# Optimization experiments

Hardware: AMD Instinct MI355X
Metric: run time of the kernel (lower is better)

## Reference

```python
import jax, jax.numpy as jnp
import numpy as np


def setup_inputs() -> dict:
    key = jax.random.key(0)
    k1, k2 = jax.random.split(key)
    B, N, P = 8, 16384, 2048
    xyz = jax.random.uniform(k1, (B, N, 3), dtype=jnp.float32)
    center_xyz = jax.random.uniform(k2, (B, P, 3), dtype=jnp.float32)
    return {
        "xyz": xyz,
        "center_xyz": center_xyz,
        "max_radius": jnp.float32(0.2),
        "sample_num": 32,
    }


def reference(xyz, center_xyz, max_radius, sample_num):
    # xyz: [B, N, 3], center_xyz: [B, P, 3] -> idx: [B, P, sample_num] int32
    B, P, _ = center_xyz.shape
    N = xyz.shape[1]
    S = int(sample_num)

    # squared distances via ||c||^2 + ||x||^2 - 2 c.x (avoids [B,P,N,3] temp)
    xn = jnp.sum(xyz * xyz, axis=-1)                      # [B, N]
    cn = jnp.sum(center_xyz * center_xyz, axis=-1)        # [B, P]
    dot = jnp.einsum("bpd,bnd->bpn", center_xyz, xyz)     # [B, P, N]
    d2 = cn[:, :, None] + xn[:, None, :] - 2.0 * dot       # [B, P, N]

    mask = d2 < (max_radius * max_radius)                  # dist < r  <=>  dist^2 < r^2
    # rank of each point among the valid ones (in index order), as in torch.where order
    rank = jnp.cumsum(mask.astype(jnp.int32), axis=-1) - 1 # [B, P, N]
    take = mask & (rank < S)
    # valid points write into slot=rank; everything else into dump slot S (discarded)
    slot = jnp.where(take, rank, S)                        # [B, P, N]

    buf = jnp.zeros((B, P, S + 1), dtype=jnp.int32)        # zeros match torch init fill
    bi = jnp.arange(B)[:, None, None]
    pi = jnp.arange(P)[None, :, None]
    src = jnp.broadcast_to(jnp.arange(N, dtype=jnp.int32), (B, P, N))
    buf = buf.at[bi, pi, slot].set(src)
    return buf[:, :, :S]
```

## Files before the change

kernel.cpp:

```cpp
#include <hip/hip_runtime.h>
#include <hip/hip_bf16.h>


typedef float f32x4 __attribute__((ext_vector_type(4)));

__global__ __launch_bounds__(256) void pack_points(
    const float* __restrict__ xyz,
    f32x4* __restrict__ q,
    int total)
{
    const int n = blockIdx.x * blockDim.x + threadIdx.x;
    if (n >= total) return;
    const float x = xyz[(size_t)n * 3 + 0];
    const float y = xyz[(size_t)n * 3 + 1];
    const float z = xyz[(size_t)n * 3 + 2];
    const float xn = __builtin_fmaf(z, z,
                      __builtin_fmaf(y, y, __fmul_rn(x, x)));
    f32x4 v;
    v[0] = x; v[1] = y; v[2] = z; v[3] = xn;
    q[n] = v;
}

__global__ __launch_bounds__(256) void ball_query_block(
    const f32x4* __restrict__ q,
    const float* __restrict__ center,
    const float* __restrict__ p_radius,
    const int*   __restrict__ p_sample,
    int* __restrict__ out,
    int B, int N, int P)
{
    const int S = p_sample[0];
    const float r = p_radius[0];
    const float r2 = __fmul_rn(r, r);

    const int c = blockIdx.x;
    const int lane = threadIdx.x & 63;
    const int wv = threadIdx.x >> 6;

    const int b = c / P;

    const float cx = center[(size_t)c * 3 + 0];
    const float cy = center[(size_t)c * 3 + 1];
    const float cz = center[(size_t)c * 3 + 2];
    const float cn = __builtin_fmaf(cz, cz,
                      __builtin_fmaf(cy, cy, __fmul_rn(cx, cx)));

    const f32x4* qb = q + (size_t)b * N;
    int* ob = out + (size_t)c * S;

    __shared__ int counts[2][4];

    int cnt = 0;
    int buf = 0;
    for (int n0 = 0; n0 < N; n0 += 1024) {
        const int base = n0 + wv * 256 + lane;

        f32x4 v[4];
#pragma unroll
        for (int j = 0; j < 4; ++j) {
            v[j] = qb[base + j * 64];
        }

        unsigned long long mm[4];
        int pc[4];
        int wtotal = 0;
#pragma unroll
        for (int j = 0; j < 4; ++j) {
            const float x = v[j][0], y = v[j][1], z = v[j][2];
            const float xn = v[j][3];
            const float dot = __builtin_fmaf(cz, z,
                               __builtin_fmaf(cy, y, __fmul_rn(cx, x)));
            const float d2 = __fsub_rn(__fadd_rn(cn, xn), __fmul_rn(2.0f, dot));
            mm[j] = __ballot(d2 < r2);
            pc[j] = __popcll(mm[j]);
            wtotal += pc[j];
        }

        if (lane == 0) counts[buf][wv] = wtotal;
        __syncthreads();

        const int c0 = counts[buf][0];
        const int c1 = counts[buf][1];
        const int c2 = counts[buf][2];
        const int c3 = counts[buf][3];
        int prefix = 0;
        if (wv > 0) prefix += c0;
        if (wv > 1) prefix += c1;
        if (wv > 2) prefix += c2;
        const int total = (c0 + c1) + (c2 + c3);

        if (wtotal != 0) {
            int off = cnt + prefix;
#pragma unroll
            for (int j = 0; j < 4; ++j) {
                const unsigned long long m = mm[j];
                const bool valid = (m >> lane) & 1ull;
                const int rank = __builtin_amdgcn_mbcnt_hi(
                    (unsigned)(m >> 32),
                    __builtin_amdgcn_mbcnt_lo((unsigned)m, 0u));
                const int slot = off + rank;
                if (valid && slot < S) {
                    ob[slot] = base + j * 64;
                }
                off += pc[j];
            }
        }

        cnt += total;
        buf ^= 1;
        if (cnt >= S) break;
    }

    if (cnt > S) cnt = S;
    for (int s = cnt + (int)threadIdx.x; s < S; s += 256) {
        ob[s] = 0;
    }
}

extern "C" void kernel_launch(void* const* d_in, const int* in_sizes, int n_in,
                              void* d_out, int out_size, void* d_ws, size_t ws_size,
                              hipStream_t stream) {
    const float* xyz      = (const float*)d_in[0];
    const float* center   = (const float*)d_in[1];
    const float* p_radius = (const float*)d_in[2];
    const int*   p_sample = (const int*)d_in[3];

    const int B = 8;
    const int N = in_sizes[0] / (B * 3);
    const int P = in_sizes[1] / (B * 3);

    int* out = (int*)d_out;
    f32x4* q = (f32x4*)d_ws;

    const int total = B * N;
    pack_points<<<(total + 255) / 256, 256, 0, stream>>>(xyz, q, total);

    const int blocks = B * P;
    const int threads = 256;
    ball_query_block<<<blocks, threads, 0, stream>>>(
        q, center, p_radius, p_sample, out, B, N, P);
}
```

Measured before the change: 82.51 us.

## Process eight centers per block to reuse loaded point tiles

Result: slower. 87.81 us (+6.4%).

```diff
diff --git a/kernel.cpp b/kernel.cpp
--- a/kernel.cpp
+++ b/kernel.cpp
@@ -3,6 +3,8 @@
 
 
 typedef float f32x4 __attribute__((ext_vector_type(4)));
+
+#define C 8
 
 __global__ __launch_bounds__(256) void pack_points(
     const float* __restrict__ xyz,
@@ -21,7 +23,7 @@
     q[n] = v;
 }
 
-__global__ __launch_bounds__(256) void ball_query_block(
+__global__ __launch_bounds__(256) void ball_query_multi(
     const f32x4* __restrict__ q,
     const float* __restrict__ center,
     const float* __restrict__ p_radius,
@@ -33,24 +35,31 @@
     const float r = p_radius[0];
     const float r2 = __fmul_rn(r, r);
 
-    const int c = blockIdx.x;
+    const int cbase = blockIdx.x * C;
     const int lane = threadIdx.x & 63;
     const int wv = threadIdx.x >> 6;
 
-    const int b = c / P;
+    const int b = cbase / P;
 
-    const float cx = center[(size_t)c * 3 + 0];
-    const float cy = center[(size_t)c * 3 + 1];
-    const float cz = center[(size_t)c * 3 + 2];
-    const float cn = __builtin_fmaf(cz, cz,
-                      __builtin_fmaf(cy, cy, __fmul_rn(cx, cx)));
+    float cxk[C], cyk[C], czk[C], cnk[C];
+#pragma unroll
+    for (int k = 0; k < C; ++k) {
+        const float cx = center[(size_t)(cbase + k) * 3 + 0];
+        const float cy = center[(size_t)(cbase + k) * 3 + 1];
+        const float cz = center[(size_t)(cbase + k) * 3 + 2];
+        cxk[k] = cx; cyk[k] = cy; czk[k] = cz;
+        cnk[k] = __builtin_fmaf(cz, cz,
+                  __builtin_fmaf(cy, cy, __fmul_rn(cx, cx)));
+    }
 
     const f32x4* qb = q + (size_t)b * N;
-    int* ob = out + (size_t)c * S;
 
-    __shared__ int counts[2][4];
+    __shared__ int counts[2][4][C];
 
-    int cnt = 0;
+    int cnt[C];
+#pragma unroll
+    for (int k = 0; k < C; ++k) cnt[k] = 0;
+
     int buf = 0;
     for (int n0 = 0; n0 < N; n0 += 1024) {
         const int base = n0 + wv * 256 + lane;
@@ -61,59 +70,79 @@
             v[j] = qb[base + j * 64];
         }
 
-        unsigned long long mm[4];
-        int pc[4];
-        int wtotal = 0;
+        unsigned vb[C];
+        int wtot[C];
 #pragma unroll
-        for (int j = 0; j < 4; ++j) {
-            const float x = v[j][0], y = v[j][1], z = v[j][2];
-            const float xn = v[j][3];
-            const float dot = __builtin_fmaf(cz, z,
-                               __builtin_fmaf(cy, y, __fmul_rn(cx, x)));
-            const float d2 = __fsub_rn(__fadd_rn(cn, xn), __fmul_rn(2.0f, dot));
-            mm[j] = __ballot(d2 < r2);
-            pc[j] = __popcll(mm[j]);
-            wtotal += pc[j];
+        for (int k = 0; k < C; ++k) {
+            vb[k] = 0; wtot[k] = 0;
+            if (cnt[k] >= S) continue;
+            unsigned bits = 0;
+            int t = 0;
+#pragma unroll
+            for (int j = 0; j < 4; ++j) {
+                const float x = v[j][0], y = v[j][1], z = v[j][2];
+                const float xn = v[j][3];
+                const float dot = __builtin_fmaf(czk[k], z,
+                                   __builtin_fmaf(cyk[k], y,
+                                                  __fmul_rn(cxk[k], x)));
+                const float s = __fadd_rn(cnk[k], xn);
+                const float d2 = __builtin_fmaf(-2.0f, dot, s);
+                const unsigned long long m = __ballot(d2 < r2);
+                bits |= ((unsigned)((m >> lane) & 1ull)) << j;
+                t += __popcll(m);
+            }
+            vb[k] = bits; wtot[k] = t;
         }
-
-        if (lane == 0) counts[buf][wv] = wtotal;
+        if (lane == 0) {
+#pragma unroll
+            for (int k = 0; k < C; ++k) counts[buf][wv][k] = wtot[k];
+        }
         __syncthreads();
 
-        const int c0 = counts[buf][0];
-        const int c1 = counts[buf][1];
-        const int c2 = counts[buf][2];
-        const int c3 = counts[buf][3];
-        int prefix = 0;
-        if (wv > 0) prefix += c0;
-        if (wv > 1) prefix += c1;
-        if (wv > 2) prefix += c2;
-        const int total = (c0 + c1) + (c2 + c3);
-
-        if (wtotal != 0) {
-            int off = cnt + prefix;
+        bool alldone = true;
 #pragma unroll
-            for (int j = 0; j < 4; ++j) {
-                const unsigned long long m = mm[j];
-                const bool valid = (m >> lane) & 1ull;
-                const int rank = __builtin_amdgcn_mbcnt_hi(
-                    (unsigned)(m >> 32),
-                    __builtin_amdgcn_mbcnt_lo((unsigned)m, 0u));
-                const int slot = off + rank;
-                if (valid && slot < S) {
-                    ob[slot] = base + j * 64;
+        for (int k = 0; k < C; ++k) {
+            if (cnt[k] >= S) continue;
+            const int c0 = counts[buf][0][k];
+            const int c1 = counts[buf][1][k];
+            const int c2 = counts[buf][2][k];
+            const int c3 = counts[buf][3][k];
+            const int total = (c0 + c1) + (c2 + c3);
+            if (wtot[k] != 0) {
+                int prefix = 0;
+                if (wv > 0) prefix += c0;
+                if (wv > 1) prefix += c1;
+                if (wv > 2) prefix += c2;
+                int off = cnt[k] + prefix;
+                int* ob = out + (size_t)(cbase + k) * S;
+#pragma unroll
+                for (int j = 0; j < 4; ++j) {
+                    const unsigned long long m = __ballot((vb[k] >> j) & 1u);
+                    const bool valid = (m >> lane) & 1ull;
+                    const int rank = __builtin_amdgcn_mbcnt_hi(
+                        (unsigned)(m >> 32),
+                        __builtin_amdgcn_mbcnt_lo((unsigned)m, 0u));
+                    const int slot = off + rank;
+                    if (valid && slot < S) {
+                        ob[slot] = base + j * 64;
+                    }
+                    off += __popcll(m);
                 }
-                off += pc[j];
             }
+            cnt[k] += total;
+            if (cnt[k] < S) alldone = false;
         }
-
-        cnt += total;
         buf ^= 1;
-        if (cnt >= S) break;
+        if (alldone) break;
     }
 
-    if (cnt > S) cnt = S;
-    for (int s = cnt + (int)threadIdx.x; s < S; s += 256) {
-        ob[s] = 0;
+#pragma unroll
+    for (int k = 0; k < C; ++k) {
+        int e = cnt[k] > S ? S : cnt[k];
+        int* ob = out + (size_t)(cbase + k) * S;
+        for (int s = e + (int)threadIdx.x; s < S; s += 256) {
+            ob[s] = 0;
+        }
     }
 }
 
@@ -135,8 +164,8 @@
     const int total = B * N;
     pack_points<<<(total + 255) / 256, 256, 0, stream>>>(xyz, q, total);
 
-    const int blocks = B * P;
+    const int blocks = (B * P) / C;
     const int threads = 256;
-    ball_query_block<<<blocks, threads, 0, stream>>>(
+    ball_query_multi<<<blocks, threads, 0, stream>>>(
         q, center, p_radius, p_sample, out, B, N, P);
 }
```

## Process each center with a single wavefront instead of a 256-thread block

Applied to the files above, without the earlier changes.

Result: no change. 81.15 us (-1.6%).

```diff
diff --git a/kernel.cpp b/kernel.cpp
--- a/kernel.cpp
+++ b/kernel.cpp
@@ -21,7 +21,7 @@
     q[n] = v;
 }
 
-__global__ __launch_bounds__(256) void ball_query_block(
+__global__ __launch_bounds__(64) void ball_query_wave(
     const f32x4* __restrict__ q,
     const float* __restrict__ center,
     const float* __restrict__ p_radius,
@@ -34,8 +34,7 @@
     const float r2 = __fmul_rn(r, r);
 
     const int c = blockIdx.x;
-    const int lane = threadIdx.x & 63;
-    const int wv = threadIdx.x >> 6;
+    const int lane = threadIdx.x;
 
     const int b = c / P;
 
@@ -48,71 +47,36 @@
     const f32x4* qb = q + (size_t)b * N;
     int* ob = out + (size_t)c * S;
 
-    __shared__ int counts[2][4];
-
     int cnt = 0;
-    int buf = 0;
-    for (int n0 = 0; n0 < N; n0 += 1024) {
-        const int base = n0 + wv * 256 + lane;
-
-        f32x4 v[4];
+    for (int n0 = 0; n0 < N && cnt < S; n0 += 512) {
+        f32x4 v[8];
 #pragma unroll
-        for (int j = 0; j < 4; ++j) {
-            v[j] = qb[base + j * 64];
+        for (int j = 0; j < 8; ++j) {
+            v[j] = qb[n0 + j * 64 + lane];
         }
 
-        unsigned long long mm[4];
-        int pc[4];
-        int wtotal = 0;
 #pragma unroll
-        for (int j = 0; j < 4; ++j) {
+        for (int j = 0; j < 8; ++j) {
             const float x = v[j][0], y = v[j][1], z = v[j][2];
             const float xn = v[j][3];
             const float dot = __builtin_fmaf(cz, z,
                                __builtin_fmaf(cy, y, __fmul_rn(cx, x)));
             const float d2 = __fsub_rn(__fadd_rn(cn, xn), __fmul_rn(2.0f, dot));
-            mm[j] = __ballot(d2 < r2);
-            pc[j] = __popcll(mm[j]);
-            wtotal += pc[j];
+
+            const bool valid = d2 < r2;
+            const unsigned long long m = __ballot(valid);
+            const int rank = __builtin_amdgcn_mbcnt_hi(
+                (unsigned)(m >> 32),
+                __builtin_amdgcn_mbcnt_lo((unsigned)m, 0u));
+            if (valid && (cnt + rank) < S) {
+                ob[cnt + rank] = n0 + j * 64 + lane;
+            }
+            cnt += __popcll(m);
         }
-
-        if (lane == 0) counts[buf][wv] = wtotal;
-        __syncthreads();
-
-        const int c0 = counts[buf][0];
-        const int c1 = counts[buf][1];
-        const int c2 = counts[buf][2];
-        const int c3 = counts[buf][3];
-        int prefix = 0;
-        if (wv > 0) prefix += c0;
-        if (wv > 1) prefix += c1;
-        if (wv > 2) prefix += c2;
-        const int total = (c0 + c1) + (c2 + c3);
-
-        if (wtotal != 0) {
-            int off = cnt + prefix;
-#pragma unroll
-            for (int j = 0; j < 4; ++j) {
-                const unsigned long long m = mm[j];
-                const bool valid = (m >> lane) & 1ull;
-                const int rank = __builtin_amdgcn_mbcnt_hi(
-                    (unsigned)(m >> 32),
-                    __builtin_amdgcn_mbcnt_lo((unsigned)m, 0u));
-                const int slot = off + rank;
-                if (valid && slot < S) {
-                    ob[slot] = base + j * 64;
-                }
-                off += pc[j];
-            }
-        }
-
-        cnt += total;
-        buf ^= 1;
-        if (cnt >= S) break;
     }
 
     if (cnt > S) cnt = S;
-    for (int s = cnt + (int)threadIdx.x; s < S; s += 256) {
+    for (int s = cnt + lane; s < S; s += 64) {
         ob[s] = 0;
     }
 }
@@ -136,7 +100,6 @@
     pack_points<<<(total + 255) / 256, 256, 0, stream>>>(xyz, q, total);
 
     const int blocks = B * P;
-    const int threads = 256;
-    ball_query_block<<<blocks, threads, 0, stream>>>(
+    ball_query_wave<<<blocks, 64, 0, stream>>>(
         q, center, p_radius, p_sample, out, B, N, P);
 }
```
